# Optimization experiments

Hardware: AMD Instinct MI355X
Metric: run time of the kernel (lower is better)

## Reference

```python
import jax, jax.numpy as jnp
import numpy as np

H, C = 8, 32          # heads, per-head channels (h_feats)
NEG_SLOPE = 0.2


def setup_inputs() -> dict:
    key = jax.random.key(0)
    ks = jax.random.split(key, 9)
    N, E, F_IN, F_E = 50000, 800000, 128, 16
    x = jax.random.normal(ks[0], (N, F_IN), jnp.float32)
    edge_index = jax.random.randint(ks[1], (2, E), 0, N, jnp.int64)
    edge_attr = jax.random.normal(ks[2], (E, F_E), jnp.float32)
    s = 1.0 / np.sqrt(F_IN)
    W = jax.random.normal(ks[3], (H * C, F_IN), jnp.float32) * s
    W_edge = jax.random.normal(ks[4], (H * C, F_E), jnp.float32) * (1.0 / np.sqrt(F_E))
    att_src = jax.random.normal(ks[5], (H, C), jnp.float32) * (1.0 / np.sqrt(C))
    att_dst = jax.random.normal(ks[6], (H, C), jnp.float32) * (1.0 / np.sqrt(C))
    att_edge = jax.random.normal(ks[7], (H, C), jnp.float32) * (1.0 / np.sqrt(C))
    bias = jnp.zeros((C,), jnp.float32)
    return {"x": x, "edge_index": edge_index, "edge_attr": edge_attr,
            "W": W, "W_edge": W_edge, "att_src": att_src, "att_dst": att_dst,
            "att_edge": att_edge, "bias": bias}


def reference(x, edge_index, edge_attr, W, W_edge, att_src, att_dst, att_edge, bias):
    N = x.shape[0]
    src, dst = edge_index[0], edge_index[1]

    # --- add self loops, edge_attr fill_value='mean' (per-dst mean of incoming attrs) ---
    deg = jax.ops.segment_sum(jnp.ones_like(dst, dtype=edge_attr.dtype), dst, num_segments=N)
    loop_attr = jax.ops.segment_sum(edge_attr, dst, num_segments=N) / jnp.maximum(deg, 1.0)[:, None]
    loop = jnp.arange(N, dtype=src.dtype)
    src = jnp.concatenate([src, loop])
    dst = jnp.concatenate([dst, loop])
    ea = jnp.concatenate([edge_attr, loop_attr], axis=0)  # [E+N, F_e]

    # --- node projection and per-node attention terms ---
    xh = (x @ W.T).reshape(N, H, C)                      # [N,H,C]
    a_src = jnp.einsum('nhc,hc->nh', xh, att_src)        # [N,H]
    a_dst = jnp.einsum('nhc,hc->nh', xh, att_dst)        # [N,H]

    # edge attention folded: (lin_edge(e).view(E,H,C) * att_edge).sum(-1) == e @ M
    M = jnp.einsum('hcf,hc->fh', W_edge.reshape(H, C, -1), att_edge)  # [F_e,H]
    a_edge = ea @ M                                      # [E+N,H]

    alpha = a_src[src] + a_dst[dst] + a_edge             # [E+N,H]
    alpha = jnp.where(alpha >= 0, alpha, NEG_SLOPE * alpha)

    # --- scatter-softmax over edges grouped by dst node ---
    amax = jax.ops.segment_max(alpha, dst, num_segments=N)  # every node has a self loop
    ex = jnp.exp(alpha - amax[dst])
    denom = jax.ops.segment_sum(ex, dst, num_segments=N)
    att = ex / denom[dst]                                # [E+N,H]

    # --- weighted message scatter-sum ---
    msg = xh[src] * att[..., None]                       # [E+N,H,C]
    out = jax.ops.segment_sum(msg, dst, num_segments=N)  # [N,H,C]
    return out.mean(axis=1) + bias                       # concat=False -> head mean
```

## Files before the change

### kernel.cpp

```cpp
#include <hip/hip_runtime.h>
#include <math.h>

#define H 8
#define C 32
#define HC 256
#define FE 16
#define FIN 128
#define NEG_SLOPE 0.2f

typedef __attribute__((ext_vector_type(8))) short bf16x8;
typedef __attribute__((ext_vector_type(4))) float f32x4;

__device__ __forceinline__ unsigned short f2bf(float f) {
  unsigned int u = __float_as_uint(f);
  unsigned int lsb = (u >> 16) & 1u;
  u += 0x7fffu + lsb;
  return (unsigned short)(u >> 16);
}
__device__ __forceinline__ float bf2f(unsigned short s) {
  return __uint_as_float(((unsigned int)s) << 16);
}

__device__ __forceinline__ void split8(const float* v, bf16x8& hi, bf16x8& lo) {
#pragma unroll
  for (int i = 0; i < 8; ++i) {
    unsigned int u = __float_as_uint(v[i]);
    unsigned int hu = u & 0xffff0000u;
    float r = v[i] - __uint_as_float(hu);
    hi[i] = (short)(hu >> 16);
    lo[i] = (short)f2bf(r);
  }
}

__global__ __launch_bounds__(256) void k_xh(const float* __restrict__ x,
                                            const float* __restrict__ W,
                                            const float* __restrict__ att_src,
                                            const float* __restrict__ att_dst,
                                            unsigned short* __restrict__ xhb,
                                            float* __restrict__ a_src,
                                            float* __restrict__ a_dst, int N) {
  int t = threadIdx.x;
  int w = t >> 6, lane = t & 63;
  int n15 = lane & 15, q = lane >> 4;
  int nodeBase = blockIdx.x * 128 + w * 32;
  int chBase = blockIdx.y * 128;

  f32x4 acc[8][2];
#pragma unroll
  for (int mt = 0; mt < 8; ++mt)
#pragma unroll
    for (int nt = 0; nt < 2; ++nt) acc[mt][nt] = (f32x4)(0.f);

  for (int ks = 0; ks < 4; ++ks) {
    int kOff = ks * 32 + q * 8;
    bf16x8 Bhi[2], Blo[2];
#pragma unroll
    for (int nt = 0; nt < 2; ++nt) {
      int node = nodeBase + nt * 16 + n15;
      int rn = (node < N) ? node : (N - 1);
      const float* px = &x[(size_t)rn * FIN + kOff];
      float vb[8];
      *(float4*)&vb[0] = *(const float4*)px;
      *(float4*)&vb[4] = *(const float4*)(px + 4);
      split8(vb, Bhi[nt], Blo[nt]);
    }
#pragma unroll
    for (int mt = 0; mt < 8; ++mt) {
      const float* pw = &W[(size_t)(chBase + mt * 16 + n15) * FIN + kOff];
      float va[8];
      *(float4*)&va[0] = *(const float4*)pw;
      *(float4*)&va[4] = *(const float4*)(pw + 4);
      bf16x8 Ahi, Alo;
      split8(va, Ahi, Alo);
#pragma unroll
      for (int nt = 0; nt < 2; ++nt) {
        acc[mt][nt] = __builtin_amdgcn_mfma_f32_16x16x32_bf16(Ahi, Bhi[nt], acc[mt][nt], 0, 0, 0);
        acc[mt][nt] = __builtin_amdgcn_mfma_f32_16x16x32_bf16(Ahi, Blo[nt], acc[mt][nt], 0, 0, 0);
        acc[mt][nt] = __builtin_amdgcn_mfma_f32_16x16x32_bf16(Alo, Bhi[nt], acc[mt][nt], 0, 0, 0);
      }
    }
  }

  float ps[2][4] = {{0.f,0.f,0.f,0.f},{0.f,0.f,0.f,0.f}};
  float pd[2][4] = {{0.f,0.f,0.f,0.f},{0.f,0.f,0.f,0.f}};
#pragma unroll
  for (int mt = 0; mt < 8; ++mt) {
    int hl = mt >> 1;
#pragma unroll
    for (int r = 0; r < 4; ++r) {
      int ch = chBase + mt * 16 + q * 4 + r;
      float as_c = att_src[ch], ad_c = att_dst[ch];
#pragma unroll
      for (int nt = 0; nt < 2; ++nt) {
        float val = acc[mt][nt][r];
        ps[nt][hl] = fmaf(val, as_c, ps[nt][hl]);
        pd[nt][hl] = fmaf(val, ad_c, pd[nt][hl]);
      }
    }
#pragma unroll
    for (int nt = 0; nt < 2; ++nt) {
      int node = nodeBase + nt * 16 + n15;
      if (node < N) {
        ushort4 us;
        us.x = f2bf(acc[mt][nt][0]); us.y = f2bf(acc[mt][nt][1]);
        us.z = f2bf(acc[mt][nt][2]); us.w = f2bf(acc[mt][nt][3]);
        *(ushort4*)&xhb[(size_t)node * HC + chBase + mt * 16 + q * 4] = us;
      }
    }
  }
#pragma unroll
  for (int nt = 0; nt < 2; ++nt)
#pragma unroll
    for (int hl = 0; hl < 4; ++hl) {
      ps[nt][hl] += __shfl_xor(ps[nt][hl], 16, 64);
      ps[nt][hl] += __shfl_xor(ps[nt][hl], 32, 64);
      pd[nt][hl] += __shfl_xor(pd[nt][hl], 16, 64);
      pd[nt][hl] += __shfl_xor(pd[nt][hl], 32, 64);
    }
  if (q == 0) {
#pragma unroll
    for (int nt = 0; nt < 2; ++nt) {
      int node = nodeBase + nt * 16 + n15;
      if (node < N) {
        *(float4*)&a_src[node * H + blockIdx.y * 4] = make_float4(ps[nt][0], ps[nt][1], ps[nt][2], ps[nt][3]);
        *(float4*)&a_dst[node * H + blockIdx.y * 4] = make_float4(pd[nt][0], pd[nt][1], pd[nt][2], pd[nt][3]);
      }
    }
  }
}

__global__ __launch_bounds__(256) void k_deg(const int* __restrict__ ei,
                                             int* __restrict__ deg,
                                             int* __restrict__ rank, int E) {
  int e = blockIdx.x * 256 + threadIdx.x;
  if (e < E) rank[e] = atomicAdd(&deg[ei[E + e]], 1);
}

__global__ __launch_bounds__(256) void k_scan1(const int* __restrict__ deg,
                                               int* __restrict__ bsum, int N) {
  int t = threadIdx.x;
  int i = blockIdx.x * 256 + t;
  int v = (i < N) ? deg[i] : 0;
#pragma unroll
  for (int m = 1; m < 64; m <<= 1) v += __shfl_xor(v, m, 64);
  __shared__ int wsum[4];
  if ((t & 63) == 0) wsum[t >> 6] = v;
  __syncthreads();
  if (t == 0) bsum[blockIdx.x] = wsum[0] + wsum[1] + wsum[2] + wsum[3];
}

__global__ __launch_bounds__(256) void k_scan2(const int* __restrict__ bsum,
                                               int* __restrict__ boff, int nb) {
  __shared__ int buf[256];
  int t = threadIdx.x;
  int v = (t < nb) ? bsum[t] : 0;
  buf[t] = v;
  __syncthreads();
  for (int off = 1; off < 256; off <<= 1) {
    int y = (t >= off) ? buf[t - off] : 0;
    __syncthreads();
    buf[t] += y;
    __syncthreads();
  }
  if (t < nb) boff[t] = buf[t] - v;
}

__global__ __launch_bounds__(256) void k_scan3(const int* __restrict__ deg,
                                               const int* __restrict__ boff,
                                               int* __restrict__ rowptr, int N, int E) {
  __shared__ int buf[256];
  int t = threadIdx.x;
  int i = blockIdx.x * 256 + t;
  int v = (i < N) ? deg[i] : 0;
  buf[t] = v;
  __syncthreads();
  for (int off = 1; off < 256; off <<= 1) {
    int y = (t >= off) ? buf[t - off] : 0;
    __syncthreads();
    buf[t] += y;
    __syncthreads();
  }
  if (i < N) rowptr[i] = boff[blockIdx.x] + buf[t] - v;
  if (i == 0) rowptr[N] = E;
}

__global__ __launch_bounds__(256) void k_edge_scatter(const int* __restrict__ ei,
                                                      const float* __restrict__ ea,
                                                      const float* __restrict__ W_edge,
                                                      const float* __restrict__ att_edge,
                                                      const int* __restrict__ rowptr,
                                                      const int* __restrict__ rank,
                                                      int* __restrict__ colsrc,
                                                      unsigned short* __restrict__ apre16, int E) {
  __shared__ float Ms[FE * H];
  int t = threadIdx.x;
  if (t < FE * H) {
    int f = t >> 3, h = t & 7;
    float acc = 0.f;
#pragma unroll
    for (int c = 0; c < C; ++c)
      acc += W_edge[(h * C + c) * FE + f] * att_edge[h * C + c];
    Ms[f * H + h] = acc;
  }
  __syncthreads();
  int e = blockIdx.x * 256 + t;
  if (e >= E) return;
  int s = ei[e], d = ei[E + e];
  const float4* p = (const float4*)&ea[(size_t)e * FE];
  float4 v0 = p[0], v1 = p[1], v2 = p[2], v3 = p[3];
  float eav[FE] = {v0.x, v0.y, v0.z, v0.w, v1.x, v1.y, v1.z, v1.w,
                   v2.x, v2.y, v2.z, v2.w, v3.x, v3.y, v3.z, v3.w};
  float o[H];
#pragma unroll
  for (int h = 0; h < H; ++h) {
    float acc = 0.f;
#pragma unroll
    for (int f = 0; f < FE; ++f) acc += eav[f] * Ms[f * H + h];
    o[h] = acc;
  }
  int pos = rowptr[d] + rank[e];
  colsrc[pos] = s;
  uint4 pk;
  pk.x = (unsigned int)f2bf(o[0]) | ((unsigned int)f2bf(o[1]) << 16);
  pk.y = (unsigned int)f2bf(o[2]) | ((unsigned int)f2bf(o[3]) << 16);
  pk.z = (unsigned int)f2bf(o[4]) | ((unsigned int)f2bf(o[5]) << 16);
  pk.w = (unsigned int)f2bf(o[6]) | ((unsigned int)f2bf(o[7]) << 16);
  *(uint4*)&apre16[(size_t)pos * H] = pk;
}

__global__ __launch_bounds__(256) void k_node(const unsigned short* __restrict__ xhb,
                                              const float* __restrict__ a_src,
                                              const float* __restrict__ a_dst,
                                              const unsigned short* __restrict__ apre16,
                                              const int* __restrict__ colsrc,
                                              const int* __restrict__ rowptr,
                                              const float* __restrict__ bias,
                                              float* __restrict__ out, int N) {
  int lane = threadIdx.x & 63;
  int n = blockIdx.x * 4 + (threadIdx.x >> 6);
  if (n >= N) return;
  int start = rowptr[n];
  int deg = rowptr[n + 1] - start;
  int hc = lane >> 3;
  float adst = a_dst[n * H + hc];
  float asrc = a_src[n * H + hc];

  float m = -1e30f, l = 0.f, psum = 0.f;
  float ax = 0.f, ay = 0.f, az = 0.f, aw = 0.f;

#pragma unroll 4
  for (int j = 0; j < deg; ++j) {
    int src = colsrc[start + j];
    float ae = bf2f(apre16[(size_t)(start + j) * H + hc]);
    psum += ae;
    float al = a_src[src * H + hc] + adst + ae;
    al = (al >= 0.f) ? al : NEG_SLOPE * al;
    float nm = fmaxf(m, al);
    float s = __expf(m - nm);
    float w = __expf(al - nm);
    m = nm;
    l = fmaf(l, s, w);
    ushort4 u = *(const ushort4*)&xhb[(size_t)src * HC + lane * 4];
    ax = fmaf(ax, s, w * bf2f(u.x));
    ay = fmaf(ay, s, w * bf2f(u.y));
    az = fmaf(az, s, w * bf2f(u.z));
    aw = fmaf(aw, s, w * bf2f(u.w));
  }

  float aself = asrc + adst + psum / fmaxf((float)deg, 1.f);
  aself = (aself >= 0.f) ? aself : NEG_SLOPE * aself;
  {
    float nm = fmaxf(m, aself);
    float s = __expf(m - nm);
    float w = __expf(aself - nm);
    m = nm;
    l = fmaf(l, s, w);
    ushort4 u = *(const ushort4*)&xhb[(size_t)n * HC + lane * 4];
    ax = fmaf(ax, s, w * bf2f(u.x));
    ay = fmaf(ay, s, w * bf2f(u.y));
    az = fmaf(az, s, w * bf2f(u.z));
    aw = fmaf(aw, s, w * bf2f(u.w));
  }
  float inv = 1.f / l;
  ax *= inv; ay *= inv; az *= inv; aw *= inv;

#pragma unroll
  for (int mm = 8; mm <= 32; mm <<= 1) {
    ax += __shfl_xor(ax, mm, 64);
    ay += __shfl_xor(ay, mm, 64);
    az += __shfl_xor(az, mm, 64);
    aw += __shfl_xor(aw, mm, 64);
  }
  if (lane < 8) {
    float4 b = ((const float4*)bias)[lane];
    float4 o;
    o.x = ax * 0.125f + b.x;
    o.y = ay * 0.125f + b.y;
    o.z = az * 0.125f + b.z;
    o.w = aw * 0.125f + b.w;
    ((float4*)&out[(size_t)n * C])[lane] = o;
  }
}

extern "C" void kernel_launch(void* const* d_in, const int* in_sizes, int n_in,
                              void* d_out, int out_size, void* d_ws, size_t ws_size,
                              hipStream_t stream) {
  const float* x        = (const float*)d_in[0];
  const int*   ei       = (const int*)d_in[1];
  const float* ea       = (const float*)d_in[2];
  const float* W        = (const float*)d_in[3];
  const float* W_edge   = (const float*)d_in[4];
  const float* att_src  = (const float*)d_in[5];
  const float* att_dst  = (const float*)d_in[6];
  const float* att_edge = (const float*)d_in[7];
  const float* bias     = (const float*)d_in[8];
  float* out = (float*)d_out;

  int N = in_sizes[0] / FIN;
  int E = in_sizes[1] / 2;
  int nb = (N + 255) / 256;

  char* ws = (char*)d_ws;
  auto take = [&](size_t bytes) {
    char* p = ws;
    ws += (bytes + 255) & ~(size_t)255;
    return p;
  };
  unsigned short* xhb    = (unsigned short*)take((size_t)N * HC * 2);
  float*          a_src  = (float*)take((size_t)N * H * 4);
  float*          a_dst  = (float*)take((size_t)N * H * 4);
  unsigned short* apre16 = (unsigned short*)take((size_t)E * H * 2);
  int*            deg    = (int*)take((size_t)N * 4);
  int*            rowptr = (int*)take((size_t)(N + 1) * 4);
  int*            rank   = (int*)take((size_t)E * 4);
  int*            colsrc = (int*)take((size_t)E * 4);
  int*            bsum   = (int*)take((size_t)nb * 4);
  int*            boff   = (int*)take((size_t)nb * 4);

  hipMemsetAsync(deg, 0, (size_t)N * 4, stream);
  k_deg<<<(E + 255) / 256, 256, 0, stream>>>(ei, deg, rank, E);
  k_xh<<<dim3((N + 127) / 128, 2), 256, 0, stream>>>(x, W, att_src, att_dst, xhb, a_src, a_dst, N);
  k_scan1<<<nb, 256, 0, stream>>>(deg, bsum, N);
  k_scan2<<<1, 256, 0, stream>>>(bsum, boff, nb);
  k_scan3<<<nb, 256, 0, stream>>>(deg, boff, rowptr, N, E);
  k_edge_scatter<<<(E + 255) / 256, 256, 0, stream>>>(ei, ea, W_edge, att_edge, rowptr, rank, colsrc, apre16, E);
  k_node<<<(N + 3) / 4, 256, 0, stream>>>(xhb, a_src, a_dst, apre16, colsrc, rowptr, bias, out, N);
}
```

Before: 313.0 us.

## Two-pass edge softmax with packed edge records and pre-split bf16 weights

Splits W into bf16 hi/lo halves once in a small kernel instead of re-splitting inside every k_xh block. Packs each edge's attention logits and source index into one 32-byte record so the node kernel reads a single stream. Replaces the serial online softmax, which ran one edge per iteration, with a two-pass scheme: eight edges are processed per iteration across lanes, weights and sources are cached in LDS for the first 64 edges, and a plain weighted gather follows. This removes the per-edge rescaling and its dependency chain, at the cost of a larger edge record (32 B instead of 20 B per edge) and recomputing logits for nodes with degree above 64. An unused duplicate kernel, k_wsplit, is left in the file.

```diff
diff --git a/kernel.cpp b/kernel.cpp
--- a/kernel.cpp
+++ b/kernel.cpp
@@ -32,8 +32,31 @@
   }
 }
 
+__global__ __launch_bounds__(256) void k_wsplit(const float* __restrict__ W,
+                                                unsigned short* __restrict__ Whi,
+                                                unsigned short* __restrict__ Wlo) {
+  int i = blockIdx.x * 256 + threadIdx.x;
+  float v = W[i];
+  unsigned int u = __float_as_uint(v);
+  unsigned int hu = u & 0xffff0000u;
+  Whi[i] = (unsigned short)(hu >> 16);
+  Wlo[i] = f2bf(v - __uint_as_float(hu)) , (unsigned short)0;
+}
+
+__global__ __launch_bounds__(256) void k_wsplit2(const float* __restrict__ W,
+                                                 unsigned short* __restrict__ Whi,
+                                                 unsigned short* __restrict__ Wlo) {
+  int i = blockIdx.x * 256 + threadIdx.x;
+  float v = W[i];
+  unsigned int u = __float_as_uint(v);
+  unsigned int hu = u & 0xffff0000u;
+  Whi[i] = (unsigned short)(hu >> 16);
+  Wlo[i] = f2bf(v - __uint_as_float(hu));
+}
+
 __global__ __launch_bounds__(256) void k_xh(const float* __restrict__ x,
-                                            const float* __restrict__ W,
+                                            const unsigned short* __restrict__ Whi,
+                                            const unsigned short* __restrict__ Wlo,
                                             const float* __restrict__ att_src,
                                             const float* __restrict__ att_dst,
                                             unsigned short* __restrict__ xhb,
@@ -66,12 +89,9 @@
     }
 #pragma unroll
     for (int mt = 0; mt < 8; ++mt) {
-      const float* pw = &W[(size_t)(chBase + mt * 16 + n15) * FIN + kOff];
-      float va[8];
-      *(float4*)&va[0] = *(const float4*)pw;
-      *(float4*)&va[4] = *(const float4*)(pw + 4);
-      bf16x8 Ahi, Alo;
-      split8(va, Ahi, Alo);
+      int widx = ((chBase + mt * 16 + n15) << 7) + kOff;
+      bf16x8 Ahi = *(const bf16x8*)&Whi[widx];
+      bf16x8 Alo = *(const bf16x8*)&Wlo[widx];
 #pragma unroll
       for (int nt = 0; nt < 2; ++nt) {
         acc[mt][nt] = __builtin_amdgcn_mfma_f32_16x16x32_bf16(Ahi, Bhi[nt], acc[mt][nt], 0, 0, 0);
@@ -190,8 +210,7 @@
                                                       const float* __restrict__ att_edge,
                                                       const int* __restrict__ rowptr,
                                                       const int* __restrict__ rank,
-                                                      int* __restrict__ colsrc,
-                                                      unsigned short* __restrict__ apre16, int E) {
+                                                      unsigned short* __restrict__ recs, int E) {
   __shared__ float Ms[FE * H];
   int t = threadIdx.x;
   if (t < FE * H) {
@@ -219,85 +238,163 @@
     o[h] = acc;
   }
   int pos = rowptr[d] + rank[e];
-  colsrc[pos] = s;
   uint4 pk;
   pk.x = (unsigned int)f2bf(o[0]) | ((unsigned int)f2bf(o[1]) << 16);
   pk.y = (unsigned int)f2bf(o[2]) | ((unsigned int)f2bf(o[3]) << 16);
   pk.z = (unsigned int)f2bf(o[4]) | ((unsigned int)f2bf(o[5]) << 16);
   pk.w = (unsigned int)f2bf(o[6]) | ((unsigned int)f2bf(o[7]) << 16);
-  *(uint4*)&apre16[(size_t)pos * H] = pk;
+  uint4 hv; hv.x = (unsigned int)s; hv.y = 0; hv.z = 0; hv.w = 0;
+  unsigned short* rp = &recs[(size_t)pos * 16];
+  *(uint4*)rp = pk;
+  *(uint4*)(rp + 8) = hv;
 }
 
 __global__ __launch_bounds__(256) void k_node(const unsigned short* __restrict__ xhb,
                                               const float* __restrict__ a_src,
                                               const float* __restrict__ a_dst,
-                                              const unsigned short* __restrict__ apre16,
-                                              const int* __restrict__ colsrc,
+                                              const unsigned short* __restrict__ recs,
                                               const int* __restrict__ rowptr,
                                               const float* __restrict__ bias,
                                               float* __restrict__ out, int N) {
+  __shared__ float wlds[4][512];
+  __shared__ int   slds[4][64];
+  int wv = threadIdx.x >> 6;
   int lane = threadIdx.x & 63;
-  int n = blockIdx.x * 4 + (threadIdx.x >> 6);
+  int n = blockIdx.x * 4 + wv;
   if (n >= N) return;
   int start = rowptr[n];
   int deg = rowptr[n + 1] - start;
-  int hc = lane >> 3;
-  float adst = a_dst[n * H + hc];
-  float asrc = a_src[n * H + hc];
-
-  float m = -1e30f, l = 0.f, psum = 0.f;
-  float ax = 0.f, ay = 0.f, az = 0.f, aw = 0.f;
-
-#pragma unroll 4
-  for (int j = 0; j < deg; ++j) {
-    int src = colsrc[start + j];
-    float ae = bf2f(apre16[(size_t)(start + j) * H + hc]);
-    psum += ae;
-    float al = a_src[src * H + hc] + adst + ae;
-    al = (al >= 0.f) ? al : NEG_SLOPE * al;
-    float nm = fmaxf(m, al);
-    float s = __expf(m - nm);
-    float w = __expf(al - nm);
-    m = nm;
-    l = fmaf(l, s, w);
-    ushort4 u = *(const ushort4*)&xhb[(size_t)src * HC + lane * 4];
-    ax = fmaf(ax, s, w * bf2f(u.x));
-    ay = fmaf(ay, s, w * bf2f(u.y));
-    az = fmaf(az, s, w * bf2f(u.z));
-    aw = fmaf(aw, s, w * bf2f(u.w));
-  }
-
+  int h = lane & 7, esub = lane >> 3;
+  float adst = a_dst[n * H + h];
+  float asrc = a_src[n * H + h];
+
+  float pmax = -1e30f, psum = 0.f;
+  float a0, a1, a2, a3, a4, a5, a6, a7;
+#define PH1(IT, AV)                                                          \
+  {                                                                          \
+    int j = IT * 8 + esub;                                                   \
+    float al = -1e30f;                                                       \
+    if (j < deg) {                                                           \
+      int b = (start + j) * 16;                                              \
+      float ae = bf2f(recs[b + h]);                                          \
+      int src = *(const int*)&recs[b + 8];                                   \
+      if (h == 0) slds[wv][j] = src;                                         \
+      psum += ae;                                                            \
+      al = a_src[src * H + h] + adst + ae;                                   \
+      al = (al >= 0.f) ? al : NEG_SLOPE * al;                                \
+      pmax = fmaxf(pmax, al);                                                \
+    }                                                                        \
+    AV = al;                                                                 \
+  }
+  PH1(0, a0) PH1(1, a1) PH1(2, a2) PH1(3, a3)
+  PH1(4, a4) PH1(5, a5) PH1(6, a6) PH1(7, a7)
+#undef PH1
+  for (int j0 = 64; j0 < deg; j0 += 8) {
+    int j = j0 + esub;
+    if (j < deg) {
+      int b = (start + j) * 16;
+      float ae = bf2f(recs[b + h]);
+      int src = *(const int*)&recs[b + 8];
+      psum += ae;
+      float al = a_src[src * H + h] + adst + ae;
+      al = (al >= 0.f) ? al : NEG_SLOPE * al;
+      pmax = fmaxf(pmax, al);
+    }
+  }
+#pragma unroll
+  for (int m = 8; m <= 32; m <<= 1) {
+    pmax = fmaxf(pmax, __shfl_xor(pmax, m, 64));
+    psum += __shfl_xor(psum, m, 64);
+  }
   float aself = asrc + adst + psum / fmaxf((float)deg, 1.f);
   aself = (aself >= 0.f) ? aself : NEG_SLOPE * aself;
+  float amax = fmaxf(pmax, aself);
+
+  float den = 0.f;
+#define PH2(IT, AV)                                                          \
+  {                                                                          \
+    int j = IT * 8 + esub;                                                   \
+    if (j < deg) {                                                           \
+      float wj = __expf(AV - amax);                                          \
+      den += wj;                                                             \
+      wlds[wv][j * 8 + h] = wj;                                              \
+    }                                                                        \
+  }
+  PH2(0, a0) PH2(1, a1) PH2(2, a2) PH2(3, a3)
+  PH2(4, a4) PH2(5, a5) PH2(6, a6) PH2(7, a7)
+#undef PH2
+  for (int j0 = 64; j0 < deg; j0 += 8) {
+    int j = j0 + esub;
+    if (j < deg) {
+      int b = (start + j) * 16;
+      float ae = bf2f(recs[b + h]);
+      int src = *(const int*)&recs[b + 8];
+      float al = a_src[src * H + h] + adst + ae;
+      al = (al >= 0.f) ? al : NEG_SLOPE * al;
+      den += __expf(al - amax);
+    }
+  }
+#pragma unroll
+  for (int m = 8; m <= 32; m <<= 1) den += __shfl_xor(den, m, 64);
+  float wself = __expf(aself - amax);
+  float inv = 1.f / (den + wself);
+
+  int hc = lane >> 3;
+  float inv_c  = __shfl(inv, hc, 64);
+  float ws_c   = __shfl(wself, hc, 64);
+  float amax_c = __shfl(amax, hc, 64);
+  float adst_c = __shfl(adst, hc, 64);
+  float accx, accy, accz, accw;
   {
-    float nm = fmaxf(m, aself);
-    float s = __expf(m - nm);
-    float w = __expf(aself - nm);
-    m = nm;
-    l = fmaf(l, s, w);
-    ushort4 u = *(const ushort4*)&xhb[(size_t)n * HC + lane * 4];
-    ax = fmaf(ax, s, w * bf2f(u.x));
-    ay = fmaf(ay, s, w * bf2f(u.y));
-    az = fmaf(az, s, w * bf2f(u.z));
-    aw = fmaf(aw, s, w * bf2f(u.w));
-  }
-  float inv = 1.f / l;
-  ax *= inv; ay *= inv; az *= inv; aw *= inv;
-
-#pragma unroll
-  for (int mm = 8; mm <= 32; mm <<= 1) {
-    ax += __shfl_xor(ax, mm, 64);
-    ay += __shfl_xor(ay, mm, 64);
-    az += __shfl_xor(az, mm, 64);
-    aw += __shfl_xor(aw, mm, 64);
+    const uint2* px = (const uint2*)(xhb + (((unsigned)n) << 8));
+    uint2 u = px[lane];
+    accx = ws_c * __uint_as_float(u.x << 16);
+    accy = ws_c * __uint_as_float(u.x & 0xffff0000u);
+    accz = ws_c * __uint_as_float(u.y << 16);
+    accw = ws_c * __uint_as_float(u.y & 0xffff0000u);
+  }
+  int dlim = (deg < 64) ? deg : 64;
+#pragma unroll 2
+  for (int j = 0; j < dlim; ++j) {
+    float wj = wlds[wv][j * 8 + hc];
+    int src = slds[wv][j];
+    const uint2* p = (const uint2*)(xhb + (((unsigned)src) << 8));
+    uint2 v = p[lane];
+    accx = fmaf(__uint_as_float(v.x << 16), wj, accx);
+    accy = fmaf(__uint_as_float(v.x & 0xffff0000u), wj, accy);
+    accz = fmaf(__uint_as_float(v.y << 16), wj, accz);
+    accw = fmaf(__uint_as_float(v.y & 0xffff0000u), wj, accw);
+  }
+  for (int j = 64; j < deg; ++j) {
+    int b = (start + j) * 16;
+    float ae = bf2f(recs[b + hc]);
+    int src = *(const int*)&recs[b + 8];
+    float al = a_src[src * H + hc] + adst_c + ae;
+    al = (al >= 0.f) ? al : NEG_SLOPE * al;
+    float wj = __expf(al - amax_c);
+    const uint2* p = (const uint2*)(xhb + (((unsigned)src) << 8));
+    uint2 v = p[lane];
+    accx = fmaf(__uint_as_float(v.x << 16), wj, accx);
+    accy = fmaf(__uint_as_float(v.x & 0xffff0000u), wj, accy);
+    accz = fmaf(__uint_as_float(v.y << 16), wj, accz);
+    accw = fmaf(__uint_as_float(v.y & 0xffff0000u), wj, accw);
+  }
+  accx *= inv_c; accy *= inv_c; accz *= inv_c; accw *= inv_c;
+
+#pragma unroll
+  for (int m = 8; m <= 32; m <<= 1) {
+    accx += __shfl_xor(accx, m, 64);
+    accy += __shfl_xor(accy, m, 64);
+    accz += __shfl_xor(accz, m, 64);
+    accw += __shfl_xor(accw, m, 64);
   }
   if (lane < 8) {
     float4 b = ((const float4*)bias)[lane];
     float4 o;
-    o.x = ax * 0.125f + b.x;
-    o.y = ay * 0.125f + b.y;
-    o.z = az * 0.125f + b.z;
-    o.w = aw * 0.125f + b.w;
+    o.x = accx * 0.125f + b.x;
+    o.y = accy * 0.125f + b.y;
+    o.z = accz * 0.125f + b.z;
+    o.w = accw * 0.125f + b.w;
     ((float4*)&out[(size_t)n * C])[lane] = o;
   }
 }
@@ -329,20 +426,22 @@
   unsigned short* xhb    = (unsigned short*)take((size_t)N * HC * 2);
   float*          a_src  = (float*)take((size_t)N * H * 4);
   float*          a_dst  = (float*)take((size_t)N * H * 4);
-  unsigned short* apre16 = (unsigned short*)take((size_t)E * H * 2);
+  unsigned short* recs   = (unsigned short*)take((size_t)E * 32);
+  unsigned short* Whi    = (unsigned short*)take((size_t)HC * FIN * 2);
+  unsigned short* Wlo    = (unsigned short*)take((size_t)HC * FIN * 2);
   int*            deg    = (int*)take((size_t)N * 4);
   int*            rowptr = (int*)take((size_t)(N + 1) * 4);
   int*            rank   = (int*)take((size_t)E * 4);
-  int*            colsrc = (int*)take((size_t)E * 4);
   int*            bsum   = (int*)take((size_t)nb * 4);
   int*            boff   = (int*)take((size_t)nb * 4);
 
   hipMemsetAsync(deg, 0, (size_t)N * 4, stream);
+  k_wsplit2<<<(HC * FIN) / 256, 256, 0, stream>>>(W, Whi, Wlo);
   k_deg<<<(E + 255) / 256, 256, 0, stream>>>(ei, deg, rank, E);
-  k_xh<<<dim3((N + 127) / 128, 2), 256, 0, stream>>>(x, W, att_src, att_dst, xhb, a_src, a_dst, N);
+  k_xh<<<dim3((N + 127) / 128, 2), 256, 0, stream>>>(x, Whi, Wlo, att_src, att_dst, xhb, a_src, a_dst, N);
   k_scan1<<<nb, 256, 0, stream>>>(deg, bsum, N);
   k_scan2<<<1, 256, 0, stream>>>(bsum, boff, nb);
   k_scan3<<<nb, 256, 0, stream>>>(deg, boff, rowptr, N, E);
-  k_edge_scatter<<<(E + 255) / 256, 256, 0, stream>>>(ei, ea, W_edge, att_edge, rowptr, rank, colsrc, apre16, E);
-  k_node<<<(N + 3) / 4, 256, 0, stream>>>(xhb, a_src, a_dst, apre16, colsrc, rowptr, bias, out, N);
-}
+  k_edge_scatter<<<(E + 255) / 256, 256, 0, stream>>>(ei, ea, W_edge, att_edge, rowptr, rank, recs, E);
+  k_node<<<(N + 3) / 4, 256, 0, stream>>>(xhb, a_src, a_dst, recs, rowptr, bias, out, N);
+}
```

Result: no change. 307.0 us (-1.9%).
